# Performance work log

Measured on AMD Instinct MI355X. Metric: run time of the kernel, lower is better.

The kernel has to match this reference:

```python
import jax, jax.numpy as jnp
import numpy as np


def setup_inputs() -> dict:
    key0 = jax.random.key(0)
    kq, kk, kv = jax.random.split(key0, 3)
    B, S, E = 4, 2048, 1024
    query = jax.random.normal(kq, (B, S, E), dtype=jnp.float32)
    key = jax.random.normal(kk, (B, S, E), dtype=jnp.float32)
    value = jax.random.normal(kv, (B, S, E), dtype=jnp.float32)
    attn_mask = jnp.zeros((B, S, S), dtype=jnp.float32)
    return {"query": query, "key": key, "value": value, "attn_mask": attn_mask}


def reference(query, key, value, attn_mask):
    # qk = Q K^T / sqrt(E) + mask; softmax over last dim; dropout is
    # identity in eval mode (reference baseline); out = attn @ V.
    E = query.shape[-1]
    scale = 1.0 / jnp.sqrt(jnp.asarray(E, dtype=query.dtype))
    qk = jnp.einsum("bqe,bke->bqk", query, key) * scale + attn_mask
    attn = jax.nn.softmax(qk, axis=-1)
    out = jnp.einsum("bqk,bke->bqe", attn, value)
    return out
```

## Files before the change

### kernel.cpp

```cpp
#include <hip/hip_runtime.h>
#include <stdint.h>
#include <math.h>

typedef unsigned short u16;
typedef short bf16x8 __attribute__((ext_vector_type(8)));
typedef unsigned short u16x8 __attribute__((ext_vector_type(8)));
typedef unsigned short u16x4 __attribute__((ext_vector_type(4)));
typedef float f32x4 __attribute__((ext_vector_type(4)));

typedef __attribute__((address_space(1))) const void gvoid;
typedef __attribute__((address_space(3))) void lvoid;

#define LOG2E 1.4426950408889634f

__device__ __forceinline__ float bf2f(u16 u) {
  union { unsigned int i; float f; } v; v.i = ((unsigned int)u) << 16; return v.f;
}
__device__ __forceinline__ u16 f2bf(float f) {
  union { float ff; unsigned int i; } v; v.ff = f;
  unsigned int x = v.i;
  return (u16)((x + 0x7FFFu + ((x >> 16) & 1u)) >> 16);
}

__global__ __launch_bounds__(256)
void cvt_f32_bf16(const float* __restrict__ src, u16* __restrict__ dst, long n)
{
  long i = ((long)blockIdx.x * 256 + threadIdx.x) * 8;
  if (i + 8 > n) return;
  f32x4 a = *(const f32x4*)&src[i];
  f32x4 b = *(const f32x4*)&src[i + 4];
  u16x8 o;
#pragma unroll
  for (int j = 0; j < 4; j++) { o[j] = f2bf(a[j]); o[4 + j] = f2bf(b[j]); }
  *(u16x8*)&dst[i] = o;
}

__global__ __launch_bounds__(256)
void transcvt_v(const float* __restrict__ V, u16* __restrict__ VT, int S, int E)
{
  __shared__ u16 t[64][72];
  const int b = blockIdx.z;
  const float* Vb = V + (long)b * S * E;
  u16* VTb = VT + (long)b * S * E;
  const int k0 = blockIdx.x * 64, n0 = blockIdx.y * 64;
  const int tid = threadIdx.x;
#pragma unroll
  for (int p = 0; p < 2; p++) {
    int kk = p * 32 + (tid >> 3);
    int nn = (tid & 7) * 8;
    f32x4 a = *(const f32x4*)&Vb[(long)(k0 + kk) * E + n0 + nn];
    f32x4 c = *(const f32x4*)&Vb[(long)(k0 + kk) * E + n0 + nn + 4];
#pragma unroll
    for (int j = 0; j < 4; j++) { t[nn + j][kk] = f2bf(a[j]); t[nn + 4 + j][kk] = f2bf(c[j]); }
  }
  __syncthreads();
#pragma unroll
  for (int p = 0; p < 2; p++) {
    int nn = p * 32 + (tid >> 3);
    int kk = (tid & 7) * 8;
    u16x8 u;
#pragma unroll
    for (int j = 0; j < 8; j++) u[j] = t[nn][kk + j];
    *(u16x8*)&VTb[(long)(n0 + nn) * S + k0 + kk] = u;
  }
}

template<int HASMASK, int COUT>
__global__ __launch_bounds__(256, 3)
void gemm_bt_fast(const u16* __restrict__ A, int lda, long aRowOff,
                  const u16* __restrict__ B, int ldb, long bBatchStride,
                  void* __restrict__ Cp, int ldc, long cRowOff,
                  const float* __restrict__ maskf,
                  int K, float scale, long g0, int S, int nbx)
{
  const int tid  = threadIdx.x;
  const int lane = tid & 63;
  const int wave = tid >> 6;

  const int nwg  = gridDim.x;
  const int orig = blockIdx.x;
  const int q = nwg >> 3, r = nwg & 7;
  const int xcd = orig & 7, slot = orig >> 3;
  const int wgid = (xcd < r ? xcd * (q + 1) : r * (q + 1) + (xcd - r) * q) + slot;
  const int by = wgid / nbx;
  const int bx = wgid - by * nbx;

  const long gTile = g0 + (long)by * 128;
  const int  bidx  = (int)(gTile / S);
  const int  nTile = bx * 128;

  __shared__ u16 As[128][32];
  __shared__ u16 Bs[128][32];

  const u16* Ab = A + (gTile - aRowOff) * (long)lda;
  const u16* Bb = B + (long)bidx * bBatchStride + (long)nTile * ldb;

  const int qm = (wave >> 1) * 64;
  const int qn = (wave & 1) * 64;
  const int lm  = lane & 15;
  const int lkB = (lane >> 4) * 16;

  const int sr = lane >> 2;
  const int sc = (lane & 3) * 8;

  f32x4 acc[4][4];
#pragma unroll
  for (int i = 0; i < 4; i++)
#pragma unroll
    for (int j = 0; j < 4; j++) acc[i][j] = (f32x4){0.f, 0.f, 0.f, 0.f};

  for (int k0 = 0; k0 < K; k0 += 32) {
#pragma unroll
    for (int p = 0; p < 2; p++) {
      const int chunk = wave * 2 + p;
      const int rr = chunk * 16 + sr;
      __builtin_amdgcn_global_load_lds(
          (gvoid*)&Ab[(long)rr * lda + k0 + sc],
          (lvoid*)((char*)&As[0][0] + chunk * 1024),
          16, 0, 0);
      __builtin_amdgcn_global_load_lds(
          (gvoid*)&Bb[(long)rr * ldb + k0 + sc],
          (lvoid*)((char*)&Bs[0][0] + chunk * 1024),
          16, 0, 0);
    }
    __syncthreads();

    bf16x8 af[4], bfr[4];
#pragma unroll
    for (int rt = 0; rt < 4; rt++)
      af[rt] = *(const bf16x8*)((const char*)&As[qm + rt * 16 + lm][0] + lkB);
#pragma unroll
    for (int ct = 0; ct < 4; ct++)
      bfr[ct] = *(const bf16x8*)((const char*)&Bs[qn + ct * 16 + lm][0] + lkB);

#pragma unroll
    for (int rt = 0; rt < 4; rt++)
#pragma unroll
      for (int ct = 0; ct < 4; ct++)
        acc[rt][ct] = __builtin_amdgcn_mfma_f32_16x16x32_bf16(af[rt], bfr[ct], acc[rt][ct], 0, 0, 0);
    __syncthreads();
  }

  const int lr = (lane >> 4) * 4;
#pragma unroll
  for (int rt = 0; rt < 4; rt++) {
#pragma unroll
    for (int ct = 0; ct < 4; ct++) {
      long gr = gTile + qm + rt * 16 + lr;
      int  cc = nTile + qn + ct * 16 + lm;
#pragma unroll
      for (int i = 0; i < 4; i++) {
        float v = acc[rt][ct][i] * scale;
        if (HASMASK) v += maskf[(gr + i) * (long)ldc + cc];
        if (COUT == 0)
          ((u16*)Cp)[(gr + i - cRowOff) * (long)ldc + cc] = f2bf(v);
        else
          ((float*)Cp)[(gr + i - cRowOff) * (long)ldc + cc] = v;
      }
    }
  }
}

template<int ASRC, int BSRC, int BMODE, int HASMASK, int COUT>
__global__ __launch_bounds__(256, 2)
void gemm_bt(const void* __restrict__ Ap, int lda, long aRowOff,
             const void* __restrict__ Bp, int ldb, long bBatchStride,
             void* __restrict__ Cp, int ldc, long cRowOff,
             const float* __restrict__ maskf,
             int K, float scale, long g0, int S)
{
  const int tid  = threadIdx.x;
  const int lane = tid & 63;
  const int wave = tid >> 6;
  const long gTile = g0 + (long)blockIdx.y * 128;
  const int  b     = (int)(gTile / S);
  const int  nTile = blockIdx.x * 128;

  __shared__ u16 As[128][40];
  __shared__ u16 Bs[128][40];

  const int qm = (wave >> 1) * 64;
  const int qn = (wave & 1) * 64;

  f32x4 acc[4][4];
#pragma unroll
  for (int i = 0; i < 4; i++)
#pragma unroll
    for (int j = 0; j < 4; j++) acc[i][j] = (f32x4){0.f, 0.f, 0.f, 0.f};

  const u16*   Ab = (const u16*)Ap   + (gTile - aRowOff) * (long)lda;
  const float* Af = (const float*)Ap + (gTile - aRowOff) * (long)lda;
  const u16*   Bb = (const u16*)Bp   + (long)b * bBatchStride;
  const float* Bf = (const float*)Bp + (long)b * bBatchStride;

  const int lm = lane & 15;
  const int lk = (lane >> 4) * 8;

  for (int k0 = 0; k0 < K; k0 += 32) {
    if (ASRC == 0) {
      int srow = tid >> 2, scol = (tid & 3) * 8;
#pragma unroll
      for (int p = 0; p < 2; p++) {
        int r = p * 64 + srow;
        *(u16x8*)&As[r][scol] = *(const u16x8*)&Ab[(long)r * lda + k0 + scol];
      }
    } else {
      int srow = tid >> 3, scol = (tid & 7) * 4;
#pragma unroll
      for (int p = 0; p < 4; p++) {
        int r = p * 32 + srow;
        f32x4 a = *(const f32x4*)&Af[(long)r * lda + k0 + scol];
        u16x4 o;
#pragma unroll
        for (int j = 0; j < 4; j++) o[j] = f2bf(a[j]);
        *(u16x4*)&As[r][scol] = o;
      }
    }
    if (BMODE == 0) {
      if (BSRC == 0) {
        int srow = tid >> 2, scol = (tid & 3) * 8;
#pragma unroll
        for (int p = 0; p < 2; p++) {
          int r = p * 64 + srow;
          *(u16x8*)&Bs[r][scol] = *(const u16x8*)&Bb[(long)(nTile + r) * ldb + k0 + scol];
        }
      } else {
        int srow = tid >> 3, scol = (tid & 7) * 4;
#pragma unroll
        for (int p = 0; p < 4; p++) {
          int r = p * 32 + srow;
          f32x4 a = *(const f32x4*)&Bf[(long)(nTile + r) * ldb + k0 + scol];
          u16x4 o;
#pragma unroll
          for (int j = 0; j < 4; j++) o[j] = f2bf(a[j]);
          *(u16x4*)&Bs[r][scol] = o;
        }
      }
    }
    __syncthreads();

    bf16x8 af[4], bfr[4];
#pragma unroll
    for (int rt = 0; rt < 4; rt++)
      af[rt] = *(const bf16x8*)&As[qm + rt * 16 + lm][lk];
    if (BMODE == 0) {
#pragma unroll
      for (int ct = 0; ct < 4; ct++)
        bfr[ct] = *(const bf16x8*)&Bs[qn + ct * 16 + lm][lk];
    } else {
#pragma unroll
      for (int ct = 0; ct < 4; ct++) {
        const float* vp = Bf + (long)(k0 + lk) * ldb + nTile + qn + ct * 16 + lm;
#pragma unroll
        for (int j = 0; j < 8; j++) bfr[ct][j] = (short)f2bf(vp[(long)j * ldb]);
      }
    }
#pragma unroll
    for (int rt = 0; rt < 4; rt++)
#pragma unroll
      for (int ct = 0; ct < 4; ct++)
        acc[rt][ct] = __builtin_amdgcn_mfma_f32_16x16x32_bf16(af[rt], bfr[ct], acc[rt][ct], 0, 0, 0);
    __syncthreads();
  }

  const int lr = (lane >> 4) * 4;
#pragma unroll
  for (int rt = 0; rt < 4; rt++) {
#pragma unroll
    for (int ct = 0; ct < 4; ct++) {
      long gr = gTile + qm + rt * 16 + lr;
      int  cc = nTile + qn + ct * 16 + lm;
#pragma unroll
      for (int i = 0; i < 4; i++) {
        float v = acc[rt][ct][i] * scale;
        if (HASMASK) v += maskf[(gr + i) * (long)ldc + cc];
        if (COUT == 0)
          ((u16*)Cp)[(gr + i - cRowOff) * (long)ldc + cc] = f2bf(v);
        else
          ((float*)Cp)[(gr + i - cRowOff) * (long)ldc + cc] = v;
      }
    }
  }
}

__global__ __launch_bounds__(256)
void softmax_rows(u16* __restrict__ Sbuf, int ncols)
{
  const long row = blockIdx.x;
  u16* rp = Sbuf + row * (long)ncols;
  const int tid = threadIdx.x;

  u16x8 u = *(const u16x8*)&rp[tid * 8];
  float x[8];
  float m = -3.0e38f;
#pragma unroll
  for (int i = 0; i < 8; i++) { x[i] = bf2f(u[i]); m = fmaxf(m, x[i]); }
#pragma unroll
  for (int off = 32; off; off >>= 1) m = fmaxf(m, __shfl_xor(m, off, 64));
  __shared__ float redm[4];
  if ((tid & 63) == 0) redm[tid >> 6] = m;
  __syncthreads();
  m = fmaxf(fmaxf(redm[0], redm[1]), fmaxf(redm[2], redm[3]));

  float e[8];
  float s = 0.f;
#pragma unroll
  for (int i = 0; i < 8; i++) { e[i] = exp2f((x[i] - m) * LOG2E); s += e[i]; }
#pragma unroll
  for (int off = 32; off; off >>= 1) s += __shfl_xor(s, off, 64);
  __shared__ float reds[4];
  if ((tid & 63) == 0) reds[tid >> 6] = s;
  __syncthreads();
  s = reds[0] + reds[1] + reds[2] + reds[3];

  float inv = 1.0f / s;
  u16x8 o;
#pragma unroll
  for (int i = 0; i < 8; i++) o[i] = f2bf(e[i] * inv);
  *(u16x8*)&rp[tid * 8] = o;
}

extern "C" void kernel_launch(void* const* d_in, const int* in_sizes, int n_in,
                              void* d_out, int out_size, void* d_ws, size_t ws_size,
                              hipStream_t stream)
{
  const float* Q    = (const float*)d_in[0];
  const float* Km   = (const float*)d_in[1];
  const float* V    = (const float*)d_in[2];
  const float* mask = (const float*)d_in[3];
  float* out = (float*)d_out;

  const long qsz = in_sizes[0];
  const long msz = in_sizes[3];
  const long E = 1024;
  const long S = (msz / qsz) * E;
  const long B = qsz / (S * E);
  const long G = B * S;
  const float scale = 1.0f / sqrtf((float)E);

  const size_t convBytes = (size_t)(3 * qsz) * 2;
  const size_t rowBytes  = (size_t)S * 2;
  char* w = (char*)d_ws;
  size_t avail = ws_size;
  const bool haveConv = (ws_size >= convBytes + 128 * rowBytes);

  u16 *Qb = nullptr, *Kb = nullptr, *VTb = nullptr;
  if (haveConv) {
    Qb  = (u16*)w;              w += (size_t)qsz * 2;
    Kb  = (u16*)w;              w += (size_t)qsz * 2;
    VTb = (u16*)w;              w += (size_t)qsz * 2;
    avail -= convBytes;
  }
  long Rmax = (long)((avail / rowBytes) / 128) * 128;
  if (Rmax > G) Rmax = G;
  if (Rmax < 128) Rmax = 128;
  u16* Sbuf = (u16*)w;

  if (haveConv) {
    cvt_f32_bf16<<<dim3((unsigned)(qsz / 2048)), 256, 0, stream>>>(Q, Qb, qsz);
    cvt_f32_bf16<<<dim3((unsigned)(qsz / 2048)), 256, 0, stream>>>(Km, Kb, qsz);
    transcvt_v<<<dim3(S / 64, E / 64, B), 256, 0, stream>>>(V, VTb, (int)S, (int)E);
  }

  for (long g0 = 0; g0 < G; g0 += Rmax) {
    const long R = (G - g0 < Rmax) ? (G - g0) : Rmax;
    if (haveConv) {
      const int nbx1 = (int)(S / 128);
      gemm_bt_fast<1, 0><<<dim3((unsigned)(nbx1 * (R / 128))), 256, 0, stream>>>(
          Qb, (int)E, 0L, Kb, (int)E, S * E,
          Sbuf, (int)S, g0, mask, (int)E, scale, g0, (int)S, nbx1);
    } else {
      gemm_bt<1, 1, 0, 1, 0><<<dim3(S / 128, R / 128), 256, 0, stream>>>(
          Q, (int)E, 0L, Km, (int)E, S * E,
          Sbuf, (int)S, g0, mask, (int)E, scale, g0, (int)S);
    }
    softmax_rows<<<dim3(R), 256, 0, stream>>>(Sbuf, (int)S);
    if (haveConv) {
      const int nbx2 = (int)(E / 128);
      gemm_bt_fast<0, 1><<<dim3((unsigned)(nbx2 * (R / 128))), 256, 0, stream>>>(
          Sbuf, (int)S, g0, VTb, (int)S, E * S,
          out, (int)E, 0L, nullptr, (int)S, 1.0f, g0, (int)S, nbx2);
    } else {
      gemm_bt<0, 1, 1, 0, 1><<<dim3(E / 128, R / 128), 256, 0, stream>>>(
          Sbuf, (int)S, g0, V, (int)E, S * E,
          out, (int)E, 0L, nullptr, (int)S, 1.0f, g0, (int)S);
    }
  }
}
```

Before: 288.9 us.

## Add single-pass workspace path reusing Q buffer for V^T and drop XCD remap

Adds a fast path used when the workspace can hold bf16 Q and K plus the full score matrix. The whole computation then runs as one QK^T GEMM, one softmax and one PV GEMM with no row chunking, and the bf16 Q buffer is reused for transposed V, which is converted after the first GEMM. It also removes the XCD-aware workgroup remapping and returns to a plain 2D grid. That may lose L2 locality across the chiplets.

Result: slower. 296.6 us (+2.7%).

```diff
diff --git a/kernel.cpp b/kernel.cpp
--- a/kernel.cpp
+++ b/kernel.cpp
@@ -71,23 +71,14 @@
                   const u16* __restrict__ B, int ldb, long bBatchStride,
                   void* __restrict__ Cp, int ldc, long cRowOff,
                   const float* __restrict__ maskf,
-                  int K, float scale, long g0, int S, int nbx)
+                  int K, float scale, long g0, int S)
 {
   const int tid  = threadIdx.x;
   const int lane = tid & 63;
   const int wave = tid >> 6;
-
-  const int nwg  = gridDim.x;
-  const int orig = blockIdx.x;
-  const int q = nwg >> 3, r = nwg & 7;
-  const int xcd = orig & 7, slot = orig >> 3;
-  const int wgid = (xcd < r ? xcd * (q + 1) : r * (q + 1) + (xcd - r) * q) + slot;
-  const int by = wgid / nbx;
-  const int bx = wgid - by * nbx;
-
-  const long gTile = g0 + (long)by * 128;
+  const long gTile = g0 + (long)blockIdx.y * 128;
   const int  bidx  = (int)(gTile / S);
-  const int  nTile = bx * 128;
+  const int  nTile = blockIdx.x * 128;
 
   __shared__ u16 As[128][32];
   __shared__ u16 Bs[128][32];
@@ -113,13 +104,13 @@
 #pragma unroll
     for (int p = 0; p < 2; p++) {
       const int chunk = wave * 2 + p;
-      const int rr = chunk * 16 + sr;
+      const int r = chunk * 16 + sr;
       __builtin_amdgcn_global_load_lds(
-          (gvoid*)&Ab[(long)rr * lda + k0 + sc],
+          (gvoid*)&Ab[(long)r * lda + k0 + sc],
           (lvoid*)((char*)&As[0][0] + chunk * 1024),
           16, 0, 0);
       __builtin_amdgcn_global_load_lds(
-          (gvoid*)&Bb[(long)rr * ldb + k0 + sc],
+          (gvoid*)&Bb[(long)r * ldb + k0 + sc],
           (lvoid*)((char*)&Bs[0][0] + chunk * 1024),
           16, 0, 0);
     }
@@ -338,6 +329,31 @@
   const long G = B * S;
   const float scale = 1.0f / sqrtf((float)E);
 
+  const size_t mergedBytes = (size_t)(2 * qsz) * 2 + (size_t)G * S * 2;
+  if (ws_size >= mergedBytes) {
+    char* w = (char*)d_ws;
+    u16* Qb   = (u16*)w;
+    u16* Kb   = (u16*)(w + (size_t)qsz * 2);
+    u16* Sbuf = (u16*)(w + (size_t)(2 * qsz) * 2);
+    u16* VTb  = Qb;
+
+    cvt_f32_bf16<<<dim3((unsigned)(qsz / 2048)), 256, 0, stream>>>(Q, Qb, qsz);
+    cvt_f32_bf16<<<dim3((unsigned)(qsz / 2048)), 256, 0, stream>>>(Km, Kb, qsz);
+
+    gemm_bt_fast<1, 0><<<dim3(S / 128, G / 128), 256, 0, stream>>>(
+        Qb, (int)E, 0L, Kb, (int)E, S * E,
+        Sbuf, (int)S, 0L, mask, (int)E, scale, 0L, (int)S);
+
+    softmax_rows<<<dim3((unsigned)G), 256, 0, stream>>>(Sbuf, (int)S);
+
+    transcvt_v<<<dim3(S / 64, E / 64, B), 256, 0, stream>>>(V, VTb, (int)S, (int)E);
+
+    gemm_bt_fast<0, 1><<<dim3(E / 128, G / 128), 256, 0, stream>>>(
+        Sbuf, (int)S, 0L, VTb, (int)S, E * S,
+        out, (int)E, 0L, nullptr, (int)S, 1.0f, 0L, (int)S);
+    return;
+  }
+
   const size_t convBytes = (size_t)(3 * qsz) * 2;
   const size_t rowBytes  = (size_t)S * 2;
   char* w = (char*)d_ws;
@@ -365,10 +381,9 @@
   for (long g0 = 0; g0 < G; g0 += Rmax) {
     const long R = (G - g0 < Rmax) ? (G - g0) : Rmax;
     if (haveConv) {
-      const int nbx1 = (int)(S / 128);
-      gemm_bt_fast<1, 0><<<dim3((unsigned)(nbx1 * (R / 128))), 256, 0, stream>>>(
+      gemm_bt_fast<1, 0><<<dim3(S / 128, R / 128), 256, 0, stream>>>(
           Qb, (int)E, 0L, Kb, (int)E, S * E,
-          Sbuf, (int)S, g0, mask, (int)E, scale, g0, (int)S, nbx1);
+          Sbuf, (int)S, g0, mask, (int)E, scale, g0, (int)S);
     } else {
       gemm_bt<1, 1, 0, 1, 0><<<dim3(S / 128, R / 128), 256, 0, stream>>>(
           Q, (int)E, 0L, Km, (int)E, S * E,
@@ -376,10 +391,9 @@
     }
     softmax_rows<<<dim3(R), 256, 0, stream>>>(Sbuf, (int)S);
     if (haveConv) {
-      const int nbx2 = (int)(E / 128);
-      gemm_bt_fast<0, 1><<<dim3((unsigned)(nbx2 * (R / 128))), 256, 0, stream>>>(
+      gemm_bt_fast<0, 1><<<dim3(E / 128, R / 128), 256, 0, stream>>>(
           Sbuf, (int)S, g0, VTb, (int)S, E * S,
-          out, (int)E, 0L, nullptr, (int)S, 1.0f, g0, (int)S, nbx2);
+          out, (int)E, 0L, nullptr, (int)S, 1.0f, g0, (int)S);
     } else {
       gemm_bt<0, 1, 1, 0, 1><<<dim3(E / 128, R / 128), 256, 0, stream>>>(
           Sbuf, (int)S, g0, V, (int)E, S * E,
```
